# Performance work log

Measured on AMD Instinct MI355X. Metric: run time of the kernel, lower is better.

## Reference

```python
import jax, jax.numpy as jnp
import numpy as np

N_NODES = 100000


def setup_inputs() -> dict:
    key = jax.random.key(0)
    k1, k2, k3 = jax.random.split(key, 3)
    in_feat = jax.random.normal(k1, (N_NODES, 32), dtype=jnp.float32)
    src = jax.random.randint(k2, (1600000,), 0, N_NODES, dtype=jnp.int64)
    dst = jax.random.randint(k3, (1600000,), 0, N_NODES, dtype=jnp.int64)
    return {"in_feat": in_feat, "src": src, "dst": dst}


def reference(in_feat, src, dst):
    # DGL GraphConv, norm='both', weight=False, bias=False,
    # allow_zero_in_degree=True:
    #   h   = x * out_deg^{-1/2}            (per source node)
    #   agg = sum over edges (src -> dst) of h[src]
    #   out = agg * in_deg^{-1/2}           (per destination node)
    n = in_feat.shape[0]
    ones = jnp.ones(src.shape[0], dtype=in_feat.dtype)
    out_deg = jax.ops.segment_sum(ones, src, num_segments=n)
    in_deg = jax.ops.segment_sum(ones, dst, num_segments=n)
    # clamp degree to min 1 (DGL uses th.clamp(degs, min=1))
    out_norm = jax.lax.rsqrt(jnp.maximum(out_deg, 1.0))  # [N]
    in_norm = jax.lax.rsqrt(jnp.maximum(in_deg, 1.0))    # [N]
    h = in_feat * out_norm[:, None]                       # [N, F]
    msg = h[src]                                          # [E, F] gather
    agg = jax.ops.segment_sum(msg, dst, num_segments=n)   # [N, F] scatter-add
    return agg * in_norm[:, None]
```

## Files before the change

kernel.cpp:

```cpp
#include <hip/hip_runtime.h>

#define F 32

#define TSB 128
#define TSB_SH 7
#define NBMAX 1024
#define RND 8192
#define PT 512
#define GT 512
#define TEDGE 2560

#define SPAN 16384
#define BPG 32

#define PREP_LDS 18944

__global__ void init_kernel(int* __restrict__ out_deg, int* __restrict__ gcur,
                            int N, int NB, int C) {
    int i = blockIdx.x * blockDim.x + threadIdx.x;
    int stride = gridDim.x * blockDim.x;
    for (int j = i; j < N; j += stride) out_deg[j] = 0;
    if (i < NBMAX) gcur[i] = i * C;
}

__global__ __launch_bounds__(PT) void prep_kernel(const int* __restrict__ src,
                                                  const int* __restrict__ dst,
                                                  int* __restrict__ gcur,
                                                  unsigned* __restrict__ gbuf,
                                                  int* __restrict__ out_deg,
                                                  int E, int N, int C, int nbin) {
    __shared__ int lds[PREP_LDS];
    int t = threadIdx.x;
    int bid = blockIdx.x;

    if (bid < nbin) {
        int* cnt    = lds;
        int* off2   = lds + NBMAX;
        int* aux    = lds + 2 * NBMAX;
        int* stag_d = lds + 2 * NBMAX + PT;
        int* stag_s = stag_d + RND;
        int base = bid * RND;
        int tot = min(RND, E - base);
        if (tot <= 0) return;
        for (int j = t; j < NBMAX; j += PT) cnt[j] = 0;
        __syncthreads();
        for (int j = t; j < tot; j += PT)
            atomicAdd(&cnt[dst[base + j] >> TSB_SH], 1);
        __syncthreads();
        int c0 = cnt[2 * t], c1 = cnt[2 * t + 1];
        aux[t] = c0 + c1;
        __syncthreads();
        for (int o = 1; o < PT; o <<= 1) {
            int v = (t >= o) ? aux[t - o] : 0;
            __syncthreads();
            aux[t] += v;
            __syncthreads();
        }
        int eb = t ? aux[t - 1] : 0;
        cnt[2 * t]     = eb;      off2[2 * t]     = eb;
        cnt[2 * t + 1] = eb + c0; off2[2 * t + 1] = eb + c0;
        __syncthreads();
        for (int j = t; j < tot; j += PT) {
            int d = dst[base + j];
            int s = src[base + j];
            int pos = atomicAdd(&cnt[d >> TSB_SH], 1);
            stag_d[pos] = d;
            stag_s[pos] = s;
        }
        __syncthreads();
        for (int b = t; b < NBMAX; b += PT) {
            int c = cnt[b] - off2[b];
            if (c > 0) {
                int g = atomicAdd(&gcur[b], c);
                off2[b] = g - off2[b];
            }
        }
        __syncthreads();
        for (int i = t; i < tot; i += PT) {
            int d = stag_d[i];
            int bkt = d >> TSB_SH;
            int pos = off2[bkt] + i;
            if (pos < (bkt + 1) * C) {
                unsigned entry = ((unsigned)(d & (TSB - 1)) << 17) | (unsigned)stag_s[i];
                gbuf[pos] = entry;
            }
        }
    } else {
        int* hist = lds;
        int hbid = bid - nbin;
        int grp = hbid / BPG;
        int q   = hbid % BPG;
        int lo  = grp * SPAN;
        int sp  = min(SPAN, N - lo);
        if (sp <= 0) return;
        for (int j = t; j < SPAN; j += PT) hist[j] = 0;
        __syncthreads();
        int nvec = E >> 2;
        const int4* s4 = (const int4*)src;
        for (int i = q * PT + t; i < nvec; i += BPG * PT) {
            int4 v = s4[i];
            unsigned a;
            a = (unsigned)(v.x - lo); if (a < (unsigned)sp) atomicAdd(&hist[a], 1);
            a = (unsigned)(v.y - lo); if (a < (unsigned)sp) atomicAdd(&hist[a], 1);
            a = (unsigned)(v.z - lo); if (a < (unsigned)sp) atomicAdd(&hist[a], 1);
            a = (unsigned)(v.w - lo); if (a < (unsigned)sp) atomicAdd(&hist[a], 1);
        }
        if (q == 0) {
            int idx = (nvec << 2) + t;
            if (idx < E) {
                unsigned a = (unsigned)(src[idx] - lo);
                if (a < (unsigned)sp) atomicAdd(&hist[a], 1);
            }
        }
        __syncthreads();
        for (int j = t; j < sp; j += PT) {
            int v = hist[j];
            if (v) atomicAdd(&out_deg[lo + j], v);
        }
    }
}

__global__ __launch_bounds__(GT) void sort_gather(const float* __restrict__ x,
                                                  const int* __restrict__ out_deg,
                                                  const unsigned* __restrict__ gbuf,
                                                  const int* __restrict__ gcur,
                                                  float* __restrict__ out,
                                                  int N, int C) {
    __shared__ unsigned sbuf[TEDGE];
    __shared__ int cnt[TSB];
    __shared__ int seg[TSB];
    __shared__ int indeg[TSB];
    int t = threadIdx.x;
    int b = blockIdx.x;
    int lo = b << TSB_SH;
    int sp = min(TSB, N - lo);
    int start = b * C;
    int total = min(gcur[b] - start, C);
    int ga = t >> 3;
    int l  = t & 7;
    const float4* x4 = (const float4*)x;

    float4 acc0 = make_float4(0.f, 0.f, 0.f, 0.f);
    float4 acc1 = make_float4(0.f, 0.f, 0.f, 0.f);
    if (t < TSB) indeg[t] = 0;
    __syncthreads();

    for (int tile = 0; tile < total; tile += TEDGE) {
        int n = min(TEDGE, total - tile);
        unsigned ev[TEDGE / GT];
        int nm = 0;
        #pragma unroll
        for (int k = 0; k < TEDGE / GT; ++k) {
            int j = t + k * GT;
            if (j < n) { ev[k] = gbuf[start + tile + j]; nm = k + 1; }
        }
        if (t < TSB) cnt[t] = 0;
        __syncthreads();
        #pragma unroll
        for (int k = 0; k < TEDGE / GT; ++k)
            if (k < nm) atomicAdd(&cnt[ev[k] >> 17], 1);
        __syncthreads();
        if (t < TSB) indeg[t] += cnt[t];
        __syncthreads();
        if (t < 64) {
            int c0 = cnt[2 * t], c1 = cnt[2 * t + 1];
            int p = c0 + c1;
            #pragma unroll
            for (int o = 1; o < 64; o <<= 1) {
                int v = __shfl_up(p, o, 64);
                if (t >= o) p += v;
            }
            int excl = p - (c0 + c1);
            seg[2 * t] = excl;          cnt[2 * t] = excl;
            seg[2 * t + 1] = excl + c0; cnt[2 * t + 1] = excl + c0;
        }
        __syncthreads();
        #pragma unroll
        for (int k = 0; k < TEDGE / GT; ++k)
            if (k < nm) {
                unsigned e = ev[k];
                int pos = atomicAdd(&cnt[e >> 17], 1);
                sbuf[pos] = e;
            }
        __syncthreads();
        #pragma unroll
        for (int half = 0; half < 2; ++half) {
            int g = ga + half * 64;
            float4 a = half ? acc1 : acc0;
            int i = seg[g];
            int send = cnt[g];
            for (; i + 8 <= send; i += 8) {
                unsigned es[8]; int ds[8]; float4 vs[8];
                #pragma unroll
                for (int k = 0; k < 8; ++k) es[k] = sbuf[i + k] & 0x1FFFFu;
                #pragma unroll
                for (int k = 0; k < 8; ++k) ds[k] = out_deg[es[k]];
                #pragma unroll
                for (int k = 0; k < 8; ++k) vs[k] = x4[(size_t)es[k] * 8 + l];
                #pragma unroll
                for (int k = 0; k < 8; ++k) {
                    float c = rsqrtf((float)(ds[k] > 1 ? ds[k] : 1));
                    a.x += vs[k].x * c;
                    a.y += vs[k].y * c;
                    a.z += vs[k].z * c;
                    a.w += vs[k].w * c;
                }
            }
            for (; i < send; ++i) {
                unsigned s = sbuf[i] & 0x1FFFFu;
                int d = out_deg[s];
                float c = rsqrtf((float)(d > 1 ? d : 1));
                float4 v = x4[(size_t)s * 8 + l];
                a.x += v.x * c; a.y += v.y * c;
                a.z += v.z * c; a.w += v.w * c;
            }
            if (half) acc1 = a; else acc0 = a;
        }
        __syncthreads();
    }

    #pragma unroll
    for (int half = 0; half < 2; ++half) {
        int g = ga + half * 64;
        if (g < sp) {
            float4 a = half ? acc1 : acc0;
            int dg = indeg[g];
            float inn = rsqrtf((float)(dg > 1 ? dg : 1));
            a.x *= inn; a.y *= inn; a.z *= inn; a.w *= inn;
            *reinterpret_cast<float4*>(&out[(size_t)(lo + g) * F + l * 4]) = a;
        }
    }
}


__global__ void deg_kernel(const int* __restrict__ src, const int* __restrict__ dst,
                           int* __restrict__ out_deg, int* __restrict__ in_deg, int E) {
    int i = blockIdx.x * blockDim.x + threadIdx.x;
    if (i < E) {
        atomicAdd(&out_deg[src[i]], 1);
        atomicAdd(&in_deg[dst[i]], 1);
    }
}

__global__ void norm_kernel(const int* __restrict__ deg, float* __restrict__ norm, int n) {
    int i = blockIdx.x * blockDim.x + threadIdx.x;
    if (i < n) {
        int d = deg[i];
        norm[i] = rsqrtf((float)(d > 1 ? d : 1));
    }
}

__global__ void alloc_kernel(const int* __restrict__ in_deg, int* __restrict__ cursor,
                             int* __restrict__ counter, int N) {
    int i = blockIdx.x * blockDim.x + threadIdx.x;
    if (i < N) cursor[i] = atomicAdd(counter, in_deg[i]);
}

__global__ void fill_kernel(const int* __restrict__ src, const int* __restrict__ dst,
                            int* __restrict__ cursor, int* __restrict__ edge_src, int E) {
    int i = blockIdx.x * blockDim.x + threadIdx.x;
    if (i < E) {
        int d = dst[i];
        int slot = atomicAdd(&cursor[d], 1);
        edge_src[slot] = src[i];
    }
}

__global__ void gather_kernel(const float* __restrict__ x,
                              const int* __restrict__ edge_src,
                              const int* __restrict__ cursor_end,
                              const int* __restrict__ in_deg,
                              const float* __restrict__ out_norm,
                              float* __restrict__ out, int N) {
    int t = blockIdx.x * blockDim.x + threadIdx.x;
    int g = t >> 3, l = t & 7;
    if (g >= N) return;
    int deg = in_deg[g];
    int end = cursor_end[g];
    int beg = end - deg;
    float4 acc = make_float4(0.f, 0.f, 0.f, 0.f);
    for (int j = beg; j < end; ++j) {
        int s = edge_src[j];
        float c = out_norm[s];
        float4 v = *reinterpret_cast<const float4*>(&x[s * F + l * 4]);
        acc.x += v.x * c; acc.y += v.y * c; acc.z += v.z * c; acc.w += v.w * c;
    }
    float innorm = rsqrtf((float)(deg > 1 ? deg : 1));
    acc.x *= innorm; acc.y *= innorm; acc.z *= innorm; acc.w *= innorm;
    *reinterpret_cast<float4*>(&out[g * F + l * 4]) = acc;
}

extern "C" void kernel_launch(void* const* d_in, const int* in_sizes, int n_in,
                              void* d_out, int out_size, void* d_ws, size_t ws_size,
                              hipStream_t stream) {
    const float* x  = (const float*)d_in[0];
    const int* src  = (const int*)d_in[1];
    const int* dst  = (const int*)d_in[2];
    float* out      = (float*)d_out;

    const int N = in_sizes[0] / F;
    const int E = in_sizes[1];
    const int NB = (N + TSB - 1) / TSB;

    int C = (E + NB - 1) / NB + 512;
    C = (C + 3) & ~3;
    if (C < 64) C = 64;

    size_t need = ((size_t)N + NBMAX + (size_t)NB * C) * 4;

    if (ws_size >= need && N <= (1 << 17) && NB <= NBMAX && C <= TEDGE) {
        int* out_deg  = (int*)d_ws;
        int* gcur     = out_deg + N;
        unsigned* gbuf = (unsigned*)(gcur + NBMAX);

        int nbin = (E + RND - 1) / RND;
        int G = (N + SPAN - 1) / SPAN;
        int grid = nbin + G * BPG;

        init_kernel<<<128, 256, 0, stream>>>(out_deg, gcur, N, NB, C);
        prep_kernel<<<grid, PT, 0, stream>>>(src, dst, gcur, gbuf, out_deg,
                                             E, N, C, nbin);
        sort_gather<<<NB, GT, 0, stream>>>(x, out_deg, gbuf, gcur, out, N, C);
        return;
    }

    size_t need3 = ((size_t)3 * N + 1 + (size_t)E) * sizeof(int);
    int* out_deg = (int*)d_ws;
    int* in_deg  = out_deg + N;
    if (ws_size >= need3) {
        int* counter  = in_deg + N;
        int* cursor   = counter + 1;
        int* edge_src = cursor + N;
        hipMemsetAsync(d_ws, 0, ((size_t)2 * N + 1) * sizeof(int), stream);
        deg_kernel<<<(E + 255) / 256, 256, 0, stream>>>(src, dst, out_deg, in_deg, E);
        norm_kernel<<<(N + 255) / 256, 256, 0, stream>>>(out_deg, (float*)out_deg, N);
        alloc_kernel<<<(N + 255) / 256, 256, 0, stream>>>(in_deg, cursor, counter, N);
        fill_kernel<<<(E + 255) / 256, 256, 0, stream>>>(src, dst, cursor, edge_src, E);
        gather_kernel<<<(N * 8 + 255) / 256, 256, 0, stream>>>(
            x, edge_src, cursor, in_deg, (const float*)out_deg, out, N);
    }
}
```

Measured before the change: 72.91 us.

## Fuse init, prep and gather into one cooperative persistent kernel

Combines the three-kernel pipeline into a single cooperative kernel with grid-wide syncs between init, binning/histogram, and gather phases, with a fallback to the old launches on failure. The aim is to remove kernel launch gaps. In exchange, the gather phase runs with the prep kernel's large LDS allocation, which lowers occupancy, and it loops over buckets with a fixed grid of 512 blocks, which may leave load imbalance.

After: 176.2 us. +141.7%, slower.

```diff
diff --git a/kernel.cpp b/kernel.cpp
--- a/kernel.cpp
+++ b/kernel.cpp
@@ -1,4 +1,7 @@
 #include <hip/hip_runtime.h>
+#include <hip/hip_cooperative_groups.h>
+
+namespace cg = cooperative_groups;
 
 #define F 32
 
@@ -6,14 +9,230 @@
 #define TSB_SH 7
 #define NBMAX 1024
 #define RND 8192
-#define PT 512
-#define GT 512
+#define MT 512
 #define TEDGE 2560
+#define GRID_BLOCKS 512
 
 #define SPAN 16384
 #define BPG 32
 
 #define PREP_LDS 18944
+
+__global__ __launch_bounds__(MT) void mega_kernel(
+    const float* __restrict__ x, const int* __restrict__ src,
+    const int* __restrict__ dst, int* __restrict__ out_deg,
+    int* __restrict__ gcur, unsigned* __restrict__ gbuf,
+    float* __restrict__ out, int E, int N, int NB, int C,
+    int nbin, int nhist) {
+    __shared__ int lds[PREP_LDS];
+    cg::grid_group grid = cg::this_grid();
+    const int t = threadIdx.x;
+    const int bid = blockIdx.x;
+    const int nblk = gridDim.x;
+
+    for (int j = bid * MT + t; j < N; j += nblk * MT) out_deg[j] = 0;
+    {
+        int gtid = bid * MT + t;
+        if (gtid < NBMAX) gcur[gtid] = gtid * C;
+    }
+    grid.sync();
+
+    if (bid < nbin) {
+        int* cnt    = lds;
+        int* off2   = lds + NBMAX;
+        int* aux    = lds + 2 * NBMAX;
+        int* stag_d = lds + 2 * NBMAX + MT;
+        int* stag_s = stag_d + RND;
+        int base = bid * RND;
+        int tot = min(RND, E - base);
+        if (tot > 0) {
+            for (int j = t; j < NBMAX; j += MT) cnt[j] = 0;
+            __syncthreads();
+            for (int j = t; j < tot; j += MT)
+                atomicAdd(&cnt[dst[base + j] >> TSB_SH], 1);
+            __syncthreads();
+            int c0 = cnt[2 * t], c1 = cnt[2 * t + 1];
+            aux[t] = c0 + c1;
+            __syncthreads();
+            for (int o = 1; o < MT; o <<= 1) {
+                int v = (t >= o) ? aux[t - o] : 0;
+                __syncthreads();
+                aux[t] += v;
+                __syncthreads();
+            }
+            int eb = t ? aux[t - 1] : 0;
+            cnt[2 * t]     = eb;      off2[2 * t]     = eb;
+            cnt[2 * t + 1] = eb + c0; off2[2 * t + 1] = eb + c0;
+            __syncthreads();
+            for (int j = t; j < tot; j += MT) {
+                int d = dst[base + j];
+                int s = src[base + j];
+                int pos = atomicAdd(&cnt[d >> TSB_SH], 1);
+                stag_d[pos] = d;
+                stag_s[pos] = s;
+            }
+            __syncthreads();
+            for (int b = t; b < NBMAX; b += MT) {
+                int c = cnt[b] - off2[b];
+                if (c > 0) {
+                    int g = atomicAdd(&gcur[b], c);
+                    off2[b] = g - off2[b];
+                }
+            }
+            __syncthreads();
+            for (int i = t; i < tot; i += MT) {
+                int d = stag_d[i];
+                int bkt = d >> TSB_SH;
+                int pos = off2[bkt] + i;
+                if (pos < (bkt + 1) * C) {
+                    unsigned entry = ((unsigned)(d & (TSB - 1)) << 17) | (unsigned)stag_s[i];
+                    gbuf[pos] = entry;
+                }
+            }
+        }
+    } else if (bid - nbin < nhist) {
+        int* hist = lds;
+        int hbid = bid - nbin;
+        int grp = hbid / BPG;
+        int q   = hbid % BPG;
+        int lo  = grp * SPAN;
+        int sp  = min(SPAN, N - lo);
+        if (sp > 0) {
+            for (int j = t; j < SPAN; j += MT) hist[j] = 0;
+            __syncthreads();
+            int nvec = E >> 2;
+            const int4* s4 = (const int4*)src;
+            for (int i = q * MT + t; i < nvec; i += BPG * MT) {
+                int4 v = s4[i];
+                unsigned a;
+                a = (unsigned)(v.x - lo); if (a < (unsigned)sp) atomicAdd(&hist[a], 1);
+                a = (unsigned)(v.y - lo); if (a < (unsigned)sp) atomicAdd(&hist[a], 1);
+                a = (unsigned)(v.z - lo); if (a < (unsigned)sp) atomicAdd(&hist[a], 1);
+                a = (unsigned)(v.w - lo); if (a < (unsigned)sp) atomicAdd(&hist[a], 1);
+            }
+            if (q == 0) {
+                int idx = (nvec << 2) + t;
+                if (idx < E) {
+                    unsigned a = (unsigned)(src[idx] - lo);
+                    if (a < (unsigned)sp) atomicAdd(&hist[a], 1);
+                }
+            }
+            __syncthreads();
+            for (int j = t; j < sp; j += MT) {
+                int v = hist[j];
+                if (v) atomicAdd(&out_deg[lo + j], v);
+            }
+        }
+    }
+    grid.sync();
+
+    unsigned* sbuf = (unsigned*)lds;
+    int* cnt   = lds + TEDGE;
+    int* seg   = cnt + TSB;
+    int* indeg = seg + TSB;
+    const float4* x4 = (const float4*)x;
+    int ga = t >> 3;
+    int l  = t & 7;
+
+    for (int b = bid; b < NB; b += nblk) {
+        int lo = b << TSB_SH;
+        int sp = min(TSB, N - lo);
+        int start = b * C;
+        int total = min(gcur[b] - start, C);
+        float4 acc0 = make_float4(0.f, 0.f, 0.f, 0.f);
+        float4 acc1 = make_float4(0.f, 0.f, 0.f, 0.f);
+        if (t < TSB) indeg[t] = 0;
+        __syncthreads();
+
+        for (int tile = 0; tile < total; tile += TEDGE) {
+            int n = min(TEDGE, total - tile);
+            unsigned ev[TEDGE / MT];
+            int nm = 0;
+            #pragma unroll
+            for (int k = 0; k < TEDGE / MT; ++k) {
+                int j = t + k * MT;
+                if (j < n) { ev[k] = gbuf[start + tile + j]; nm = k + 1; }
+            }
+            if (t < TSB) cnt[t] = 0;
+            __syncthreads();
+            #pragma unroll
+            for (int k = 0; k < TEDGE / MT; ++k)
+                if (k < nm) atomicAdd(&cnt[ev[k] >> 17], 1);
+            __syncthreads();
+            if (t < TSB) indeg[t] += cnt[t];
+            __syncthreads();
+            if (t < 64) {
+                int c0 = cnt[2 * t], c1 = cnt[2 * t + 1];
+                int p = c0 + c1;
+                #pragma unroll
+                for (int o = 1; o < 64; o <<= 1) {
+                    int v = __shfl_up(p, o, 64);
+                    if (t >= o) p += v;
+                }
+                int excl = p - (c0 + c1);
+                seg[2 * t] = excl;          cnt[2 * t] = excl;
+                seg[2 * t + 1] = excl + c0; cnt[2 * t + 1] = excl + c0;
+            }
+            __syncthreads();
+            #pragma unroll
+            for (int k = 0; k < TEDGE / MT; ++k)
+                if (k < nm) {
+                    unsigned e = ev[k];
+                    int pos = atomicAdd(&cnt[e >> 17], 1);
+                    sbuf[pos] = e;
+                }
+            __syncthreads();
+            #pragma unroll
+            for (int half = 0; half < 2; ++half) {
+                int g = ga + half * 64;
+                float4 a = half ? acc1 : acc0;
+                int i = seg[g];
+                int send = cnt[g];
+                for (; i + 8 <= send; i += 8) {
+                    unsigned es[8]; int ds[8]; float4 vs[8];
+                    #pragma unroll
+                    for (int k = 0; k < 8; ++k) es[k] = sbuf[i + k] & 0x1FFFFu;
+                    #pragma unroll
+                    for (int k = 0; k < 8; ++k) ds[k] = out_deg[es[k]];
+                    #pragma unroll
+                    for (int k = 0; k < 8; ++k) vs[k] = x4[(size_t)es[k] * 8 + l];
+                    #pragma unroll
+                    for (int k = 0; k < 8; ++k) {
+                        float c = rsqrtf((float)(ds[k] > 1 ? ds[k] : 1));
+                        a.x += vs[k].x * c;
+                        a.y += vs[k].y * c;
+                        a.z += vs[k].z * c;
+                        a.w += vs[k].w * c;
+                    }
+                }
+                for (; i < send; ++i) {
+                    unsigned s = sbuf[i] & 0x1FFFFu;
+                    int d = out_deg[s];
+                    float c = rsqrtf((float)(d > 1 ? d : 1));
+                    float4 v = x4[(size_t)s * 8 + l];
+                    a.x += v.x * c; a.y += v.y * c;
+                    a.z += v.z * c; a.w += v.w * c;
+                }
+                if (half) acc1 = a; else acc0 = a;
+            }
+            __syncthreads();
+        }
+
+        #pragma unroll
+        for (int half = 0; half < 2; ++half) {
+            int g = ga + half * 64;
+            if (g < sp) {
+                float4 a = half ? acc1 : acc0;
+                int dg = indeg[g];
+                float inn = rsqrtf((float)(dg > 1 ? dg : 1));
+                a.x *= inn; a.y *= inn; a.z *= inn; a.w *= inn;
+                *reinterpret_cast<float4*>(&out[(size_t)(lo + g) * F + l * 4]) = a;
+            }
+        }
+        __syncthreads();
+    }
+}
+
 
 __global__ void init_kernel(int* __restrict__ out_deg, int* __restrict__ gcur,
                             int N, int NB, int C) {
@@ -23,7 +242,7 @@
     if (i < NBMAX) gcur[i] = i * C;
 }
 
-__global__ __launch_bounds__(PT) void prep_kernel(const int* __restrict__ src,
+__global__ __launch_bounds__(MT) void prep_kernel(const int* __restrict__ src,
                                                   const int* __restrict__ dst,
                                                   int* __restrict__ gcur,
                                                   unsigned* __restrict__ gbuf,
@@ -32,25 +251,24 @@
     __shared__ int lds[PREP_LDS];
     int t = threadIdx.x;
     int bid = blockIdx.x;
-
     if (bid < nbin) {
         int* cnt    = lds;
         int* off2   = lds + NBMAX;
         int* aux    = lds + 2 * NBMAX;
-        int* stag_d = lds + 2 * NBMAX + PT;
+        int* stag_d = lds + 2 * NBMAX + MT;
         int* stag_s = stag_d + RND;
         int base = bid * RND;
         int tot = min(RND, E - base);
         if (tot <= 0) return;
-        for (int j = t; j < NBMAX; j += PT) cnt[j] = 0;
-        __syncthreads();
-        for (int j = t; j < tot; j += PT)
+        for (int j = t; j < NBMAX; j += MT) cnt[j] = 0;
+        __syncthreads();
+        for (int j = t; j < tot; j += MT)
             atomicAdd(&cnt[dst[base + j] >> TSB_SH], 1);
         __syncthreads();
         int c0 = cnt[2 * t], c1 = cnt[2 * t + 1];
         aux[t] = c0 + c1;
         __syncthreads();
-        for (int o = 1; o < PT; o <<= 1) {
+        for (int o = 1; o < MT; o <<= 1) {
             int v = (t >= o) ? aux[t - o] : 0;
             __syncthreads();
             aux[t] += v;
@@ -60,7 +278,7 @@
         cnt[2 * t]     = eb;      off2[2 * t]     = eb;
         cnt[2 * t + 1] = eb + c0; off2[2 * t + 1] = eb + c0;
         __syncthreads();
-        for (int j = t; j < tot; j += PT) {
+        for (int j = t; j < tot; j += MT) {
             int d = dst[base + j];
             int s = src[base + j];
             int pos = atomicAdd(&cnt[d >> TSB_SH], 1);
@@ -68,7 +286,7 @@
             stag_s[pos] = s;
         }
         __syncthreads();
-        for (int b = t; b < NBMAX; b += PT) {
+        for (int b = t; b < NBMAX; b += MT) {
             int c = cnt[b] - off2[b];
             if (c > 0) {
                 int g = atomicAdd(&gcur[b], c);
@@ -76,7 +294,7 @@
             }
         }
         __syncthreads();
-        for (int i = t; i < tot; i += PT) {
+        for (int i = t; i < tot; i += MT) {
             int d = stag_d[i];
             int bkt = d >> TSB_SH;
             int pos = off2[bkt] + i;
@@ -93,11 +311,11 @@
         int lo  = grp * SPAN;
         int sp  = min(SPAN, N - lo);
         if (sp <= 0) return;
-        for (int j = t; j < SPAN; j += PT) hist[j] = 0;
+        for (int j = t; j < SPAN; j += MT) hist[j] = 0;
         __syncthreads();
         int nvec = E >> 2;
         const int4* s4 = (const int4*)src;
-        for (int i = q * PT + t; i < nvec; i += BPG * PT) {
+        for (int i = q * MT + t; i < nvec; i += BPG * MT) {
             int4 v = s4[i];
             unsigned a;
             a = (unsigned)(v.x - lo); if (a < (unsigned)sp) atomicAdd(&hist[a], 1);
@@ -113,14 +331,14 @@
             }
         }
         __syncthreads();
-        for (int j = t; j < sp; j += PT) {
+        for (int j = t; j < sp; j += MT) {
             int v = hist[j];
             if (v) atomicAdd(&out_deg[lo + j], v);
         }
     }
 }
 
-__global__ __launch_bounds__(GT) void sort_gather(const float* __restrict__ x,
+__global__ __launch_bounds__(MT) void sort_gather(const float* __restrict__ x,
                                                   const int* __restrict__ out_deg,
                                                   const unsigned* __restrict__ gbuf,
                                                   const int* __restrict__ gcur,
@@ -147,17 +365,17 @@
 
     for (int tile = 0; tile < total; tile += TEDGE) {
         int n = min(TEDGE, total - tile);
-        unsigned ev[TEDGE / GT];
+        unsigned ev[TEDGE / MT];
         int nm = 0;
         #pragma unroll
-        for (int k = 0; k < TEDGE / GT; ++k) {
-            int j = t + k * GT;
+        for (int k = 0; k < TEDGE / MT; ++k) {
+            int j = t + k * MT;
             if (j < n) { ev[k] = gbuf[start + tile + j]; nm = k + 1; }
         }
         if (t < TSB) cnt[t] = 0;
         __syncthreads();
         #pragma unroll
-        for (int k = 0; k < TEDGE / GT; ++k)
+        for (int k = 0; k < TEDGE / MT; ++k)
             if (k < nm) atomicAdd(&cnt[ev[k] >> 17], 1);
         __syncthreads();
         if (t < TSB) indeg[t] += cnt[t];
@@ -176,7 +394,7 @@
         }
         __syncthreads();
         #pragma unroll
-        for (int k = 0; k < TEDGE / GT; ++k)
+        for (int k = 0; k < TEDGE / MT; ++k)
             if (k < nm) {
                 unsigned e = ev[k];
                 int pos = atomicAdd(&cnt[e >> 17], 1);
@@ -315,12 +533,28 @@
 
         int nbin = (E + RND - 1) / RND;
         int G = (N + SPAN - 1) / SPAN;
-        int grid = nbin + G * BPG;
+        int nhist = G * BPG;
+
+        if (nbin + nhist <= GRID_BLOCKS) {
+            const float* xa = x; const int* sa = src; const int* da = dst;
+            int* oda = out_deg; int* gca = gcur; unsigned* gba = gbuf;
+            float* oa = out;
+            int Ea = E, Na = N, NBa = NB, Ca = C, nbina = nbin, nhista = nhist;
+            void* args[] = {(void*)&xa, (void*)&sa, (void*)&da, (void*)&oda,
+                            (void*)&gca, (void*)&gba, (void*)&oa, (void*)&Ea,
+                            (void*)&Na, (void*)&NBa, (void*)&Ca, (void*)&nbina,
+                            (void*)&nhista};
+            hipError_t err = hipLaunchCooperativeKernel(
+                (const void*)mega_kernel, dim3(GRID_BLOCKS), dim3(MT),
+                args, 0, stream);
+            if (err == hipSuccess) return;
+            (void)hipGetLastError();
+        }
 
         init_kernel<<<128, 256, 0, stream>>>(out_deg, gcur, N, NB, C);
-        prep_kernel<<<grid, PT, 0, stream>>>(src, dst, gcur, gbuf, out_deg,
-                                             E, N, C, nbin);
-        sort_gather<<<NB, GT, 0, stream>>>(x, out_deg, gbuf, gcur, out, N, C);
+        prep_kernel<<<nbin + nhist, MT, 0, stream>>>(src, dst, gcur, gbuf, out_deg,
+                                                     E, N, C, nbin);
+        sort_gather<<<NB, MT, 0, stream>>>(x, out_deg, gbuf, gcur, out, N, C);
         return;
     }
 
```
